# Optimization experiments

Hardware: AMD Instinct MI355X
Metric: run time of the kernel (lower is better)

## Reference

```python
import jax, jax.numpy as jnp
import numpy as np

D_MODEL = 1024
D_STATE = 16
D_CONV = 4
EXPAND = 2
D_INNER = D_MODEL * EXPAND
BATCH = 4
SEQ = 2048


def setup_inputs() -> dict:
    key = jax.random.key(0)
    ks = jax.random.split(key, 6)
    s = 0.02
    x = jax.random.normal(ks[0], (BATCH, SEQ, D_MODEL), jnp.float32)
    W_in = jax.random.normal(ks[1], (D_MODEL, 2 * D_INNER), jnp.float32) * s
    conv_w = jax.random.normal(ks[2], (D_INNER, 1, D_CONV), jnp.float32) * 0.1  # depthwise kernel (O, I/groups=1, K)
    conv_b = jnp.zeros((D_INNER,), jnp.float32)
    W_x = jax.random.normal(ks[3], (D_INNER, 2 * D_STATE), jnp.float32) * s
    W_dt = jax.random.normal(ks[4], (D_INNER, D_INNER), jnp.float32) * s
    b_dt = jnp.zeros((D_INNER,), jnp.float32)
    W_out = jax.random.normal(ks[5], (D_INNER, D_MODEL), jnp.float32) * s
    A_log = jnp.log(jnp.broadcast_to(jnp.arange(1, D_STATE + 1, dtype=jnp.float32), (D_INNER, D_STATE)))
    D_param = jnp.ones((D_INNER,), jnp.float32)
    return dict(x=x, W_in=W_in, conv_w=conv_w, conv_b=conv_b, W_x=W_x,
                W_dt=W_dt, b_dt=b_dt, W_out=W_out, A_log=A_log, D_param=D_param)


def reference(x, W_in, conv_w, conv_b, W_x, W_dt, b_dt, W_out, A_log, D_param):
    # in_proj and gate split
    xz = x @ W_in                                  # (B, L, 2*D_INNER)
    x_inner, z = jnp.split(xz, 2, axis=-1)
    # causal depthwise conv1d (torch pads both sides by d_conv-1 then slices [:L] == left pad)
    lhs = x_inner.transpose(0, 2, 1)               # (B, D_INNER, L)
    xc = jax.lax.conv_general_dilated(
        lhs, conv_w, window_strides=(1,), padding=[(D_CONV - 1, 0)],
        dimension_numbers=('NCH', 'OIH', 'NCH'), feature_group_count=D_INNER)
    xc = (xc + conv_b[None, :, None]).transpose(0, 2, 1)  # (B, L, D_INNER)
    xc = jax.nn.silu(xc)
    # input-dependent B, C, dt
    bdt = xc @ W_x                                 # (B, L, 2*D_STATE)
    B_p, C_p = jnp.split(bdt, 2, axis=-1)
    dt = jax.nn.softplus(xc @ W_dt + b_dt)         # (B, L, D_INNER)
    A = -jnp.exp(A_log)                            # (D_INNER, D_STATE)

    def step(h, ins):
        x_t, dt_t, b_t, c_t = ins                  # (B,D), (B,D), (B,N), (B,N)
        dA = jnp.exp(dt_t[..., None] * A)          # (B, D, N)
        h = dA * h + (dt_t * x_t)[..., None] * b_t[:, None, :]
        y_t = jnp.einsum('bdn,bn->bd', h, c_t)
        return h, y_t

    h0 = jnp.zeros((x.shape[0], D_INNER, D_STATE), x.dtype)
    xs = (xc.transpose(1, 0, 2), dt.transpose(1, 0, 2),
          B_p.transpose(1, 0, 2), C_p.transpose(1, 0, 2))
    _, ys = jax.lax.scan(step, h0, xs)             # (L, B, D_INNER)
    y = ys.transpose(1, 0, 2) + xc * D_param       # skip connection via D
    return (y * jax.nn.silu(z)) @ W_out            # (B, L, D_MODEL)
```

## Files before the change

### kernel.cpp

```cpp
#include <hip/hip_runtime.h>
#include <hip/hip_bf16.h>

typedef __hip_bfloat16 bf16;
typedef __attribute__((ext_vector_type(8))) short bf16x8;
typedef __attribute__((ext_vector_type(4))) float f32x4;

#define SEQ     2048
#define DMODEL  1024
#define DINNER  2048
#define NBATCH  4
#define NROWS   (NBATCH * SEQ)
#define DSTATE  16
#define NCHUNK  16
#define CHUNK   128

__device__ __forceinline__ float b2f(short s) {
    union { unsigned u; float f; } c;
    c.u = ((unsigned)(unsigned short)s) << 16;
    return c.f;
}

__device__ __forceinline__ void async16(const bf16* g, bf16* l) {
    auto gp = reinterpret_cast<const __attribute__((address_space(1))) unsigned*>(
        reinterpret_cast<uintptr_t>(g));
    auto lp = reinterpret_cast<__attribute__((address_space(3))) unsigned*>(
        reinterpret_cast<uintptr_t>(l));
    __builtin_amdgcn_global_load_lds(gp, lp, 16, 0, 0);
}

__device__ __forceinline__ void transpose_tile(
    const float* __restrict__ W, bf16* __restrict__ WT,
    int K, int N, int Npad, int bx, int by)
{
    __shared__ float tile[32][33];
    const int tx = threadIdx.x & 31, ty = threadIdx.x >> 5;
    const int x = bx * 32 + tx;
#pragma unroll
    for (int i = 0; i < 32; i += 8) {
        int y = by * 32 + ty + i;
        tile[ty + i][tx] = (x < N && y < K) ? W[(size_t)y * N + x] : 0.f;
    }
    __syncthreads();
    const int k = by * 32 + tx;
#pragma unroll
    for (int i = 0; i < 32; i += 8) {
        int n = bx * 32 + ty + i;
        if (n < Npad && k < K)
            WT[(size_t)n * K + k] = __float2bfloat16(tile[tx][ty + i]);
    }
}

__global__ __launch_bounds__(256)
void prep(const float* __restrict__ x,     const float* __restrict__ W_in,
          const float* __restrict__ W_dt,  const float* __restrict__ W_x,
          const float* __restrict__ W_out, bf16* __restrict__ x_bf,
          bf16* __restrict__ WinT, bf16* __restrict__ WcombT,
          bf16* __restrict__ WoutT)
{
    const int bid = blockIdx.x;
    if (bid < 8192) {
        int i = bid * 256 + threadIdx.x;
        float4 v = *(const float4*)(x + (size_t)i * 4);
        __align__(8) bf16 o[4] = { __float2bfloat16(v.x), __float2bfloat16(v.y),
                                   __float2bfloat16(v.z), __float2bfloat16(v.w) };
        *(uint2*)(x_bf + (size_t)i * 4) = *(uint2*)o;
    } else if (bid < 12288) {
        int t = bid - 8192;
        transpose_tile(W_in, WinT, 1024, 4096, 4096, t & 127, t >> 7);
    } else if (bid < 16384) {
        int t = bid - 12288;
        transpose_tile(W_dt, WcombT, 2048, 2048, 2048, t & 63, t >> 6);
    } else if (bid < 16640) {
        int t = bid - 16384;
        transpose_tile(W_x, WcombT + (size_t)2048 * 2048, 2048, 32, 128,
                       t & 3, t >> 2);
    } else {
        int t = bid - 16640;
        transpose_tile(W_out, WoutT, 2048, 1024, 1024, t & 31, t >> 5);
    }
}

template <int MODE>
__global__ __launch_bounds__(256, 2)
void gemm_bt(const bf16* __restrict__ A, int lda, const bf16* __restrict__ BT,
             int ldb, float* __restrict__ Cf, bf16* __restrict__ Cb, int ldc,
             const float* __restrict__ bias, int K)
{
    __shared__ __align__(16) bf16 As[2][128 * 32];
    __shared__ __align__(16) bf16 Bs[2][128 * 32];
    const int tid  = threadIdx.x;
    const int lane = tid & 63;
    const int wave = tid >> 6;

    const int gx = gridDim.x, gy = gridDim.y;
    int lin = blockIdx.y * gx + blockIdx.x;
    const int per = 8 * gx;
    int g   = lin / per;
    int rem = lin - g * per;
    int rows = min(8, gy - g * 8);
    const int by = g * 8 + rem % rows;
    const int bx = rem / rows;

    const int m0 = by * 128;
    const int n0 = bx * 128;
    const int wm = (wave & 1) * 64;
    const int wn = (wave >> 1) * 64;

    f32x4 acc[4][4];
#pragma unroll
    for (int i = 0; i < 4; ++i)
#pragma unroll
        for (int j = 0; j < 4; ++j) acc[i][j] = (f32x4){0.f, 0.f, 0.f, 0.f};

    const int c0 = wave * 128 + lane;
    const int c1 = c0 + 64;
    const int r0 = c0 >> 2, e0 = (c0 & 3) * 8;
    const int r1 = c1 >> 2, e1 = (c1 & 3) * 8;
    const bf16* pa0 = A  + (size_t)(m0 + r0) * lda + e0;
    const bf16* pa1 = A  + (size_t)(m0 + r1) * lda + e1;
    const bf16* pb0 = BT + (size_t)(n0 + r0) * ldb + e0;
    const bf16* pb1 = BT + (size_t)(n0 + r1) * ldb + e1;
    const int lw0 = wave * 1024;
    const int lw1 = wave * 1024 + 512;

    const int arow = lane & 15;
    const int akq  = (lane >> 4) * 8;
    const int KT = K >> 5;

    auto STAGE = [&](int buf, int kt) {
        const int k0 = kt * 32;
        async16(pa0 + k0, &As[buf][lw0]);
        async16(pa1 + k0, &As[buf][lw1]);
        async16(pb0 + k0, &Bs[buf][lw0]);
        async16(pb1 + k0, &Bs[buf][lw1]);
    };
    auto COMPUTE = [&](int buf) {
        bf16x8 af[4], bfr[4];
#pragma unroll
        for (int i = 0; i < 4; ++i)
            af[i] = *(const bf16x8*)(&As[buf][(wm + i * 16 + arow) * 32 + akq]);
#pragma unroll
        for (int j = 0; j < 4; ++j)
            bfr[j] = *(const bf16x8*)(&Bs[buf][(wn + j * 16 + arow) * 32 + akq]);
#pragma unroll
        for (int i = 0; i < 4; ++i)
#pragma unroll
            for (int j = 0; j < 4; ++j)
                acc[i][j] = __builtin_amdgcn_mfma_f32_16x16x32_bf16(
                    af[i], bfr[j], acc[i][j], 0, 0, 0);
    };

    STAGE(0, 0);
    __syncthreads();

    for (int kt = 0; kt < KT; kt += 2) {
        STAGE(1, kt + 1);
        COMPUTE(0);
        __syncthreads();
        if (kt + 2 < KT) STAGE(0, kt + 2);
        COMPUTE(1);
        __syncthreads();
    }

    const int rbase = (lane >> 4) * 4;
    const int cbase = lane & 15;
#pragma unroll
    for (int i = 0; i < 4; ++i) {
        int row = m0 + wm + i * 16 + rbase;
#pragma unroll
        for (int j = 0; j < 4; ++j) {
            int col = n0 + wn + j * 16 + cbase;
#pragma unroll
            for (int r = 0; r < 4; ++r) {
                float v = acc[i][j][r];
                if (MODE == 0) {
                    Cf[(size_t)(row + r) * ldc + col] = v;
                } else if (MODE == 2) {
                    Cb[(size_t)(row + r) * ldc + col] = __float2bfloat16(v);
                } else {
                    if (col < DINNER) {
                        float v2 = v + bias[col];
                        float sp = (v2 > 20.f) ? v2 : log1pf(__expf(v2));
                        Cb[(size_t)(row + r) * ldc + col] = __float2bfloat16(sp);
                    } else {
                        Cf[(size_t)(row + r) * 128 + (col - DINNER)] = v;
                    }
                }
            }
        }
    }
}

__global__ __launch_bounds__(256)
void conv_silu(const bf16* __restrict__ xz, const float* __restrict__ conv_w,
               const float* __restrict__ conv_b, bf16* __restrict__ xc)
{
    int gid = blockIdx.x * 256 + threadIdx.x;
    int d8  = gid & 255;
    int row = gid >> 8;
    int l   = row & (SEQ - 1);
    int d   = d8 * 8;
    const bf16* base = xz + (size_t)row * 4096 + d;
    float acc[8];
    float4 b0 = *(const float4*)(conv_b + d);
    float4 b1 = *(const float4*)(conv_b + d + 4);
    acc[0] = b0.x; acc[1] = b0.y; acc[2] = b0.z; acc[3] = b0.w;
    acc[4] = b1.x; acc[5] = b1.y; acc[6] = b1.z; acc[7] = b1.w;
    float w[8][4];
#pragma unroll
    for (int j = 0; j < 8; ++j) {
        float4 wv = *(const float4*)(conv_w + (size_t)(d + j) * 4);
        w[j][0] = wv.x; w[j][1] = wv.y; w[j][2] = wv.z; w[j][3] = wv.w;
    }
#pragma unroll
    for (int k = 0; k < 4; ++k) {
        if (l + k - 3 >= 0) {
            bf16x8 v = *(const bf16x8*)(base + (ptrdiff_t)(k - 3) * 4096);
#pragma unroll
            for (int j = 0; j < 8; ++j)
                acc[j] = fmaf(b2f(v[j]), w[j][k], acc[j]);
        }
    }
    __align__(16) bf16 o[8];
#pragma unroll
    for (int j = 0; j < 8; ++j) {
        float s = acc[j] / (1.f + __expf(-acc[j]));
        o[j] = __float2bfloat16(s);
    }
    *(bf16x8*)(xc + (size_t)row * DINNER + d) = *(bf16x8*)o;
}

__global__ __launch_bounds__(256)
void scan_pass1(const bf16* __restrict__ xc, const bf16* __restrict__ dt,
                const float* __restrict__ bdt, const float* __restrict__ A_log,
                float* __restrict__ P, float* __restrict__ S)
{
    const int d  = blockIdx.x * 256 + threadIdx.x;
    const int c  = blockIdx.y;
    const int b  = blockIdx.z;
    const int t0 = c * CHUNK;
    __shared__ float bls[CHUNK][DSTATE];
    for (int i = threadIdx.x; i < CHUNK * DSTATE; i += 256) {
        int tl = i >> 4, col = i & 15;
        bls[tl][col] = bdt[(size_t)(b * SEQ + t0 + tl) * 128 + col];
    }
    __syncthreads();
    float acoef[16], h[16], p[16];
#pragma unroll
    for (int n = 0; n < 16; ++n) {
        acoef[n] = -__expf(A_log[(size_t)d * 16 + n]) * 1.44269504f;
        h[n] = 0.f; p[n] = 1.f;
    }
    size_t idx = (size_t)(b * SEQ + t0) * DINNER + d;
    bf16 dcur = dt[idx], xcur = xc[idx];
    for (int tl = 0; tl < CHUNK; ++tl) {
        bf16 dnext = dcur, xnext = xcur;
        if (tl + 1 < CHUNK) {
            dnext = dt[idx + DINNER];
            xnext = xc[idx + DINNER];
        }
        float dtv = __bfloat162float(dcur);
        float xv  = __bfloat162float(xcur);
        float u = dtv * xv;
#pragma unroll
        for (int n = 0; n < 16; ++n) {
            float a = exp2f(dtv * acoef[n]);
            p[n] *= a;
            h[n] = fmaf(a, h[n], u * bls[tl][n]);
        }
        dcur = dnext; xcur = xnext; idx += DINNER;
    }
    size_t o = ((size_t)(c * NBATCH + b) * DINNER + d) * 16;
#pragma unroll
    for (int n = 0; n < 16; n += 4) {
        *(float4*)(P + o + n) = make_float4(p[n], p[n+1], p[n+2], p[n+3]);
        *(float4*)(S + o + n) = make_float4(h[n], h[n+1], h[n+2], h[n+3]);
    }
}

__global__ __launch_bounds__(256)
void scan_pass2(const float* __restrict__ P, const float* __restrict__ S,
                float* __restrict__ Hinit)
{
    size_t idx = (size_t)blockIdx.x * 256 + threadIdx.x;
    const size_t stride = (size_t)NBATCH * DINNER * 16;
    float h = 0.f;
    for (int c = 0; c < NCHUNK; ++c) {
        size_t o = (size_t)c * stride + idx;
        float p = P[o];
        float s = S[o];
        Hinit[o] = h;
        h = fmaf(p, h, s);
    }
}

__global__ __launch_bounds__(256)
void scan_pass3(const bf16* __restrict__ xc, const bf16* __restrict__ dt,
                const float* __restrict__ bdt, const float* __restrict__ A_log,
                const float* __restrict__ Hinit, const bf16* __restrict__ xzb,
                const float* __restrict__ Dp, bf16* __restrict__ U)
{
    const int d  = blockIdx.x * 256 + threadIdx.x;
    const int c  = blockIdx.y;
    const int b  = blockIdx.z;
    const int t0 = c * CHUNK;
    __shared__ float bls[CHUNK][DSTATE];
    __shared__ float cls[CHUNK][DSTATE];
    for (int i = threadIdx.x; i < CHUNK * 32; i += 256) {
        int tl = i >> 5, col = i & 31;
        float v = bdt[(size_t)(b * SEQ + t0 + tl) * 128 + col];
        if (col < 16) bls[tl][col] = v; else cls[tl][col - 16] = v;
    }
    __syncthreads();
    float acoef[16], h[16];
#pragma unroll
    for (int n = 0; n < 16; ++n)
        acoef[n] = -__expf(A_log[(size_t)d * 16 + n]) * 1.44269504f;
    size_t ho = ((size_t)(c * NBATCH + b) * DINNER + d) * 16;
#pragma unroll
    for (int n = 0; n < 16; n += 4) {
        float4 hv = *(const float4*)(Hinit + ho + n);
        h[n] = hv.x; h[n+1] = hv.y; h[n+2] = hv.z; h[n+3] = hv.w;
    }
    const float Dv = Dp[d];
    size_t idx  = (size_t)(b * SEQ + t0) * DINNER + d;
    size_t widx = (size_t)(b * SEQ + t0) * 4096 + d;
    bf16 dcur = dt[idx], xcur = xc[idx], zcur = xzb[widx + DINNER];
    for (int tl = 0; tl < CHUNK; ++tl) {
        bf16 dnext = dcur, xnext = xcur, znext = zcur;
        if (tl + 1 < CHUNK) {
            dnext = dt[idx + DINNER];
            xnext = xc[idx + DINNER];
            znext = xzb[widx + 4096 + DINNER];
        }
        float dtv = __bfloat162float(dcur);
        float xv  = __bfloat162float(xcur);
        float u = dtv * xv;
        float y = 0.f;
#pragma unroll
        for (int n = 0; n < 16; ++n) {
            float a = exp2f(dtv * acoef[n]);
            h[n] = fmaf(a, h[n], u * bls[tl][n]);
            y = fmaf(h[n], cls[tl][n], y);
        }
        float zv = __bfloat162float(zcur);
        float sz = zv / (1.f + __expf(-zv));
        float val = (y + xv * Dv) * sz;
        U[widx] = __float2bfloat16(val);
        dcur = dnext; xcur = xnext; zcur = znext;
        idx += DINNER; widx += 4096;
    }
}

extern "C" void kernel_launch(void* const* d_in, const int* in_sizes, int n_in,
                              void* d_out, int out_size, void* d_ws, size_t ws_size,
                              hipStream_t stream)
{
    const float* x      = (const float*)d_in[0];
    const float* W_in   = (const float*)d_in[1];
    const float* conv_w = (const float*)d_in[2];
    const float* conv_b = (const float*)d_in[3];
    const float* W_x    = (const float*)d_in[4];
    const float* W_dt   = (const float*)d_in[5];
    const float* b_dt   = (const float*)d_in[6];
    const float* W_out  = (const float*)d_in[7];
    const float* A_log  = (const float*)d_in[8];
    const float* Dp     = (const float*)d_in[9];
    float* out = (float*)d_out;

    char* ws = (char*)d_ws;
    size_t off = 0;
    auto alloc = [&](size_t bytes) {
        char* p = ws + off;
        off += (bytes + 255) & ~(size_t)255;
        return (void*)p;
    };
    bf16*  xzb   = (bf16*) alloc((size_t)NROWS * 4096 * 2);
    bf16*  xc    = (bf16*) alloc((size_t)NROWS * 2048 * 2);
    bf16*  dtb   = (bf16*) alloc((size_t)NROWS * 2048 * 2);
    float* bdt   = (float*)alloc((size_t)NROWS * 128 * 4);
    bf16*  WcombT= (bf16*) alloc((size_t)2176 * 2048 * 2);
    bf16*  WoutT = (bf16*) alloc((size_t)1024 * 2048 * 2);
    char*  scr   = (char*) alloc((size_t)16 << 20);
    bf16*  WinT = (bf16*)dtb;
    bf16*  x_bf = (bf16*)scr;
    float* Pb   = (float*)scr;
    float* Sb   = (float*)(scr + ((size_t)8 << 20));
    float* Hb   = Pb;
    bf16*  U    = xzb;

    prep<<<18688, 256, 0, stream>>>(x, W_in, W_dt, W_x, W_out,
                                    x_bf, WinT, WcombT, WoutT);

    gemm_bt<2><<<dim3(4096/128, NROWS/128), 256, 0, stream>>>(x_bf, 1024, WinT, 1024, nullptr, xzb, 4096, nullptr, 1024);
    conv_silu<<<(NROWS * 256) / 256, 256, 0, stream>>>(xzb, conv_w, conv_b, xc);
    gemm_bt<3><<<dim3(2176/128, NROWS/128), 256, 0, stream>>>(xc, 2048, WcombT, 2048, bdt, dtb, 2048, b_dt, 2048);
    scan_pass1<<<dim3(DINNER/256, NCHUNK, NBATCH), 256, 0, stream>>>(xc, dtb, bdt, A_log, Pb, Sb);
    scan_pass2<<<(NBATCH * DINNER * 16) / 256, 256, 0, stream>>>(Pb, Sb, Hb);
    scan_pass3<<<dim3(DINNER/256, NCHUNK, NBATCH), 256, 0, stream>>>(xc, dtb, bdt, A_log, Hb, xzb, Dp, U);
    gemm_bt<0><<<dim3(1024/128, NROWS/128), 256, 0, stream>>>(U, 4096, WoutT, 2048, out, nullptr, 1024, nullptr, 2048);
}
```

Before: 677.2 us.

## Add 256x256-tile 512-thread GEMM for input and dt/x projections

Adds a new GEMM kernel with 256x256 output tiles, a K-step of 64 and 512 threads (8 waves, each computing 128x64). It replaces the 128x128 kernel for the in_proj GEMM and the fused dt/B/C projection GEMM. The larger tile raises arithmetic intensity and cuts redundant global and LDS loads per MFMA. The combined weight buffer is padded to 2304 rows so N divides by 256; the extra rows are never written by prep and their outputs are discarded. The trade-off is 128 KB of LDS per block, which limits occupancy, plus tail imbalance with fewer, larger blocks (288 blocks for the second GEMM).

Result: slower. 738.6 us (+9.1%).

```diff
diff --git a/kernel.cpp b/kernel.cpp
--- a/kernel.cpp
+++ b/kernel.cpp
@@ -81,6 +81,120 @@
 }
 
 template <int MODE>
+__global__ __launch_bounds__(512, 2)
+void gemm256(const bf16* __restrict__ A, int lda, const bf16* __restrict__ BT,
+             int ldb, float* __restrict__ Cf, bf16* __restrict__ Cb, int ldc,
+             const float* __restrict__ bias, int K)
+{
+    __shared__ __align__(16) bf16 As[2][256 * 64];
+    __shared__ __align__(16) bf16 Bs[2][256 * 64];
+    const int tid  = threadIdx.x;
+    const int lane = tid & 63;
+    const int wave = tid >> 6;
+
+    const int gx = gridDim.x, gy = gridDim.y;
+    int lin = blockIdx.y * gx + blockIdx.x;
+    const int per = 8 * gx;
+    int g   = lin / per;
+    int rem = lin - g * per;
+    int rows = min(8, gy - g * 8);
+    const int by = g * 8 + rem % rows;
+    const int bx = rem / rows;
+
+    const int m0 = by * 256;
+    const int n0 = bx * 256;
+    const int wm = (wave >> 2) * 128;
+    const int wn = (wave & 3) * 64;
+
+    f32x4 acc[8][4];
+#pragma unroll
+    for (int i = 0; i < 8; ++i)
+#pragma unroll
+        for (int j = 0; j < 4; ++j) acc[i][j] = (f32x4){0.f, 0.f, 0.f, 0.f};
+
+    const bf16* pa[4];
+    const bf16* pb[4];
+#pragma unroll
+    for (int q = 0; q < 4; ++q) {
+        int c = q * 512 + tid;
+        int r = c >> 3, e = (c & 7) * 8;
+        pa[q] = A  + (size_t)(m0 + r) * lda + e;
+        pb[q] = BT + (size_t)(n0 + r) * ldb + e;
+    }
+
+    const int arow = lane & 15;
+    const int akq  = (lane >> 4) * 8;
+    const int KT = K >> 6;
+
+    auto STAGE = [&](int buf, int kt) {
+        const int k0 = kt * 64;
+#pragma unroll
+        for (int q = 0; q < 4; ++q)
+            async16(pa[q] + k0, &As[buf][q * 4096 + wave * 512]);
+#pragma unroll
+        for (int q = 0; q < 4; ++q)
+            async16(pb[q] + k0, &Bs[buf][q * 4096 + wave * 512]);
+    };
+    auto COMPUTE = [&](int buf) {
+#pragma unroll
+        for (int ks = 0; ks < 2; ++ks) {
+            bf16x8 bfr[4];
+#pragma unroll
+            for (int j = 0; j < 4; ++j)
+                bfr[j] = *(const bf16x8*)(
+                    &Bs[buf][(wn + j * 16 + arow) * 64 + ks * 32 + akq]);
+#pragma unroll
+            for (int i = 0; i < 8; ++i) {
+                bf16x8 af = *(const bf16x8*)(
+                    &As[buf][(wm + i * 16 + arow) * 64 + ks * 32 + akq]);
+#pragma unroll
+                for (int j = 0; j < 4; ++j)
+                    acc[i][j] = __builtin_amdgcn_mfma_f32_16x16x32_bf16(
+                        af, bfr[j], acc[i][j], 0, 0, 0);
+            }
+        }
+    };
+
+    STAGE(0, 0);
+    __syncthreads();
+
+    for (int kt = 0; kt < KT; kt += 2) {
+        STAGE(1, kt + 1);
+        COMPUTE(0);
+        __syncthreads();
+        if (kt + 2 < KT) STAGE(0, kt + 2);
+        COMPUTE(1);
+        __syncthreads();
+    }
+
+    const int rbase = (lane >> 4) * 4;
+    const int cbase = lane & 15;
+#pragma unroll
+    for (int i = 0; i < 8; ++i) {
+        int row = m0 + wm + i * 16 + rbase;
+#pragma unroll
+        for (int j = 0; j < 4; ++j) {
+            int col = n0 + wn + j * 16 + cbase;
+#pragma unroll
+            for (int r = 0; r < 4; ++r) {
+                float v = acc[i][j][r];
+                if (MODE == 2) {
+                    Cb[(size_t)(row + r) * ldc + col] = __float2bfloat16(v);
+                } else {
+                    if (col < DINNER) {
+                        float v2 = v + bias[col];
+                        float sp = (v2 > 20.f) ? v2 : log1pf(__expf(v2));
+                        Cb[(size_t)(row + r) * ldc + col] = __float2bfloat16(sp);
+                    } else if (col < DINNER + 128) {
+                        Cf[(size_t)(row + r) * 128 + (col - DINNER)] = v;
+                    }
+                }
+            }
+        }
+    }
+}
+
+template <int MODE>
 __global__ __launch_bounds__(256, 2)
 void gemm_bt(const bf16* __restrict__ A, int lda, const bf16* __restrict__ BT,
              int ldb, float* __restrict__ Cf, bf16* __restrict__ Cb, int ldc,
@@ -379,7 +493,7 @@
     bf16*  xc    = (bf16*) alloc((size_t)NROWS * 2048 * 2);
     bf16*  dtb   = (bf16*) alloc((size_t)NROWS * 2048 * 2);
     float* bdt   = (float*)alloc((size_t)NROWS * 128 * 4);
-    bf16*  WcombT= (bf16*) alloc((size_t)2176 * 2048 * 2);
+    bf16*  WcombT= (bf16*) alloc((size_t)2304 * 2048 * 2);
     bf16*  WoutT = (bf16*) alloc((size_t)1024 * 2048 * 2);
     char*  scr   = (char*) alloc((size_t)16 << 20);
     bf16*  WinT = (bf16*)dtb;
@@ -392,9 +506,9 @@
     prep<<<18688, 256, 0, stream>>>(x, W_in, W_dt, W_x, W_out,
                                     x_bf, WinT, WcombT, WoutT);
 
-    gemm_bt<2><<<dim3(4096/128, NROWS/128), 256, 0, stream>>>(x_bf, 1024, WinT, 1024, nullptr, xzb, 4096, nullptr, 1024);
+    gemm256<2><<<dim3(4096/256, NROWS/256), 512, 0, stream>>>(x_bf, 1024, WinT, 1024, nullptr, xzb, 4096, nullptr, 1024);
     conv_silu<<<(NROWS * 256) / 256, 256, 0, stream>>>(xzb, conv_w, conv_b, xc);
-    gemm_bt<3><<<dim3(2176/128, NROWS/128), 256, 0, stream>>>(xc, 2048, WcombT, 2048, bdt, dtb, 2048, b_dt, 2048);
+    gemm256<3><<<dim3(2304/256, NROWS/256), 512, 0, stream>>>(xc, 2048, WcombT, 2048, bdt, dtb, 2048, b_dt, 2048);
     scan_pass1<<<dim3(DINNER/256, NCHUNK, NBATCH), 256, 0, stream>>>(xc, dtb, bdt, A_log, Pb, Sb);
     scan_pass2<<<(NBATCH * DINNER * 16) / 256, 256, 0, stream>>>(Pb, Sb, Hb);
     scan_pass3<<<dim3(DINNER/256, NCHUNK, NBATCH), 256, 0, stream>>>(xc, dtb, bdt, A_log, Hb, xzb, Dp, U);
```
